# Kernel optimization log

Hardware: AMD Instinct MI355X
Metric: run time of the kernel (lower is better)

## Reference

```python
import jax, jax.numpy as jnp
import numpy as np

N_NODES = 30000


def gcn_conv(x, src, dst, ew, W, b, n):
    # x: [N, Fin] -> linear first (PyG GCNConv), then normalized scatter-add
    h = x @ W  # [N, Fout]
    loops = jnp.arange(n, dtype=src.dtype)
    s = jnp.concatenate([src, loops])
    d = jnp.concatenate([dst, loops])
    w = jnp.concatenate([ew, jnp.ones((n,), dtype=ew.dtype)])
    deg = jax.ops.segment_sum(w, d, num_segments=n)
    dinv = jnp.where(deg > 0, jax.lax.rsqrt(jnp.where(deg > 0, deg, 1.0)), 0.0)
    norm = dinv[s] * w * dinv[d]  # [E+N]
    msg = h[s] * norm[:, None]  # [E+N, Fout]
    out = jax.ops.segment_sum(msg, d, num_segments=n)
    return out + b


def setup_inputs() -> dict:
    key = jax.random.key(0)
    ks = jax.random.split(key, 16)
    n, e, f, c = N_NODES, 480000, 64, 64
    dims = [f, 2 * c, 4 * c, 8 * c]  # 64 -> 128 -> 256 -> 512
    num_classes = 40

    def lin(k, fi, fo):
        k1, k2 = jax.random.split(k)
        s = 1.0 / np.sqrt(fi)
        return (jax.random.uniform(k1, (fi, fo), jnp.float32, -s, s),
                jax.random.uniform(k2, (fo,), jnp.float32, -s, s))

    W1, b1 = lin(ks[0], dims[0], dims[1])
    W2, b2 = lin(ks[1], dims[1], dims[2])
    W3, b3 = lin(ks[2], dims[2], dims[3])
    fW1, fb1 = lin(ks[3], dims[3], dims[3])
    fW2, fb2 = lin(ks[4], dims[3], num_classes)
    return {
        "x": jax.random.normal(ks[5], (n, f), jnp.float32),
        "edge_index": jax.random.randint(ks[6], (2, e), 0, n, jnp.int32),
        "edge_attr": jax.random.uniform(ks[7], (e, 1), jnp.float32),
        "W1": W1, "b1": b1, "W2": W2, "b2": b2, "W3": W3, "b3": b3,
        "fW1": fW1, "fb1": fb1, "fW2": fW2, "fb2": fb2,
    }


def reference(x, edge_index, edge_attr, W1, b1, W2, b2, W3, b3, fW1, fb1, fW2, fb2):
    n = x.shape[0]
    src, dst = edge_index[0], edge_index[1]
    ew = edge_attr.squeeze(-1)
    h = jax.nn.relu(gcn_conv(x, src, dst, ew, W1, b1, n))
    h = jax.nn.relu(gcn_conv(h, src, dst, ew, W2, b2, n))
    h = jax.nn.relu(gcn_conv(h, src, dst, ew, W3, b3, n))
    h = jax.nn.relu(h @ fW1 + fb1)
    h = h @ fW2 + fb2
    return jax.nn.log_softmax(h, axis=1)
```

## Files before the change

### kernel.cpp

```cpp
#include <hip/hip_runtime.h>
#include <cstdint>
#include <cstddef>


typedef _Float16 f16;
typedef _Float16 half8 __attribute__((ext_vector_type(8)));
typedef _Float16 half4 __attribute__((ext_vector_type(4)));
typedef float v4f __attribute__((ext_vector_type(4)));
typedef unsigned long long u64;

__device__ inline void gload_lds16(const void* g, void* l) {
    __builtin_amdgcn_global_load_lds(
        (const __attribute__((address_space(1))) unsigned int*)g,
        (__attribute__((address_space(3))) unsigned int*)l, 16, 0, 0);
}


__global__ __launch_bounds__(256) void k_edge1(const int* __restrict__ dst, const float* __restrict__ ew,
                                               u64* __restrict__ packed, int* __restrict__ eslot, int E) {
    int t = blockIdx.x * blockDim.x + threadIdx.x;
    int e0 = t * 4;
    if (e0 + 3 < E) {
        int4 d4 = *(const int4*)(dst + e0);
        float4 w4 = *(const float4*)(ew + e0);
        u64 a0 = ((u64)__float2uint_rn(w4.x * 1048576.f) << 24) | 1ULL;
        u64 a1 = ((u64)__float2uint_rn(w4.y * 1048576.f) << 24) | 1ULL;
        u64 a2 = ((u64)__float2uint_rn(w4.z * 1048576.f) << 24) | 1ULL;
        u64 a3 = ((u64)__float2uint_rn(w4.w * 1048576.f) << 24) | 1ULL;
        u64 o0 = atomicAdd(&packed[d4.x], a0);
        u64 o1 = atomicAdd(&packed[d4.y], a1);
        u64 o2 = atomicAdd(&packed[d4.z], a2);
        u64 o3 = atomicAdd(&packed[d4.w], a3);
        int4 s;
        s.x = (int)(o0 & 0xFFFFFF); s.y = (int)(o1 & 0xFFFFFF);
        s.z = (int)(o2 & 0xFFFFFF); s.w = (int)(o3 & 0xFFFFFF);
        *(int4*)(eslot + e0) = s;
    } else {
        for (int e = e0; e < E; ++e) {
            u64 a = ((u64)__float2uint_rn(ew[e] * 1048576.f) << 24) | 1ULL;
            u64 o = atomicAdd(&packed[dst[e]], a);
            eslot[e] = (int)(o & 0xFFFFFF);
        }
    }
}

__global__ __launch_bounds__(256) void k_dinv_scan1(const u64* __restrict__ packed,
                                                    float* __restrict__ dinv, int* __restrict__ cnt,
                                                    int* __restrict__ bsum, int n) {
    int i = blockIdx.x * 256 + threadIdx.x;
    int c = 0;
    if (i < n) {
        u64 pk = packed[i];
        c = (int)(pk & 0xFFFFFF);
        float d = 1.0f + (float)(pk >> 24) * (1.0f / 1048576.f);
        float r = rsqrtf(d);
        r = r * (1.5f - 0.5f * d * r * r);
        dinv[i] = r;
        cnt[i] = c;
    }
    int v = c;
#pragma unroll
    for (int o = 32; o; o >>= 1) v += __shfl_xor(v, o);
    __shared__ int s[4];
    if ((threadIdx.x & 63) == 0) s[threadIdx.x >> 6] = v;
    __syncthreads();
    if (threadIdx.x == 0) bsum[blockIdx.x] = s[0] + s[1] + s[2] + s[3];
}

__device__ inline int block_scan_incl(int v) {
    __shared__ int ws[4];
    int lane = threadIdx.x & 63, w = threadIdx.x >> 6;
#pragma unroll
    for (int off = 1; off < 64; off <<= 1) {
        int t = __shfl_up(v, off);
        if (lane >= off) v += t;
    }
    if (lane == 63) ws[w] = v;
    __syncthreads();
    int add = 0;
#pragma unroll
    for (int i = 0; i < 4; ++i) add += (i < w) ? ws[i] : 0;
    __syncthreads();
    return v + add;
}

__global__ __launch_bounds__(256) void k_scan23(const int* __restrict__ cnt, const int* __restrict__ bsum,
                                                int* __restrict__ rowptr, int n, int E) {
    int blk = blockIdx.x, tid = threadIdx.x;
    int i = blk * 256 + tid;
    __shared__ int spre;
    if (tid < 64) {
        int s = 0;
        for (int j = tid; j < blk; j += 64) s += bsum[j];
#pragma unroll
        for (int o = 32; o; o >>= 1) s += __shfl_xor(s, o);
        if (tid == 0) spre = s;
    }
    __syncthreads();
    int v = (i < n) ? cnt[i] : 0;
    int incl = block_scan_incl(v);
    if (i < n) rowptr[i] = spre + incl - v;
    if (i == n - 1) rowptr[n] = E;
}

__global__ __launch_bounds__(256) void k_fill(const int* __restrict__ src, const int* __restrict__ dst,
                                              const float* __restrict__ ew, const int* __restrict__ eslot,
                                              const float* __restrict__ dinv, const int* __restrict__ rowptr,
                                              int* __restrict__ csr_src, float* __restrict__ csr_norm, int E) {
    int e = blockIdx.x * blockDim.x + threadIdx.x;
    if (e < E) {
        int d = dst[e], s = src[e];
        int idx = rowptr[d] + eslot[e];
        csr_src[idx] = s;
        csr_norm[idx] = dinv[s] * ew[e] * dinv[d];
    }
}

struct PrepArgs {
    u64* packed; int n;
    const float* x; f16* xh; int xt4;
    const float* W[5]; f16* WT[5];
    int lgK[5]; int N[5]; int off[6];
};
__global__ __launch_bounds__(256) void k_prep(PrepArgs a) {
    int i = blockIdx.x * 256 + threadIdx.x;
    if (i < a.n) { a.packed[i] = 0ULL; return; }
    int j = i - a.n;
    if (j < a.xt4) {
        float4 v = *(const float4*)(a.x + (size_t)j * 4);
        half4 h = {(f16)v.x, (f16)v.y, (f16)v.z, (f16)v.w};
        *(half4*)(a.xh + (size_t)j * 4) = h;
        return;
    }
    int w = j - a.xt4;
#pragma unroll
    for (int s = 0; s < 5; ++s) {
        if (w >= a.off[s] && w < a.off[s + 1]) {
            int li = w - a.off[s];
            int K = 1 << a.lgK[s];
            int nr = li >> a.lgK[s], k = li & (K - 1);
            float v = (nr < a.N[s]) ? a.W[s][(size_t)k * a.N[s] + nr] : 0.f;
            a.WT[s][li] = (f16)v;
        }
    }
}

template <int F>
__global__ __launch_bounds__(256) void k_agg(const f16* __restrict__ h,
                                             const float* __restrict__ dinv, const int* __restrict__ rowptr,
                                             const int* __restrict__ csr_src, const float* __restrict__ csr_norm,
                                             f16* __restrict__ o, int n) {
    constexpr int LPN = F / 8;
    constexpr int NPW = 64 / LPN;
    int wave = (int)((blockIdx.x * (unsigned)blockDim.x + threadIdx.x) >> 6);
    int lane = threadIdx.x & 63;
    int grp = lane / LPN, lin = lane % LPN;
    int node = wave * NPW + grp;
    if (node >= n) return;
    float di = dinv[node], w0 = di * di;
    float acc[8];
#pragma unroll
    for (int i = 0; i < 8; ++i) acc[i] = 0.f;

    auto gat = [&](int s, float w) {
        half8 x = *(const half8*)(h + (size_t)s * F + lin * 8);
#pragma unroll
        for (int i = 0; i < 8; ++i) acc[i] += w * (float)x[i];
    };

    gat(node, w0);
    int beg = rowptr[node], end = rowptr[node + 1];
    int j = beg;
    for (; j + 3 < end; j += 4) {
        int s0 = csr_src[j], s1 = csr_src[j + 1], s2 = csr_src[j + 2], s3 = csr_src[j + 3];
        float u0 = csr_norm[j], u1 = csr_norm[j + 1], u2 = csr_norm[j + 2], u3 = csr_norm[j + 3];
        gat(s0, u0); gat(s1, u1); gat(s2, u2); gat(s3, u3);
    }
    for (; j < end; ++j) gat(csr_src[j], csr_norm[j]);

    half8 v;
#pragma unroll
    for (int i = 0; i < 8; ++i) v[i] = (f16)acc[i];
    *(half8*)(o + (size_t)node * F + (size_t)lin * 8) = v;
}

template <bool RELU>
__global__ __launch_bounds__(256) void k_mm(const f16* __restrict__ A, const f16* __restrict__ BT,
                                            const float* __restrict__ bias, f16* __restrict__ Ch,
                                            int M, int N, int K, int nB, int nwg) {
    __shared__ f16 lsA[2][128 * 64];
    __shared__ f16 lsB[2][128 * 64];
    int wg = blockIdx.x;
    int q = nwg >> 3, r = nwg & 7;
    int xcd = wg & 7, lin = wg >> 3;
    int wgs = (xcd < r) ? (xcd * (q + 1) + lin) : (r * (q + 1) + (xcd - r) * q + lin);
    int bm = wgs / nB, bn = wgs % nB;

    int tid = threadIdx.x;
    int lane = tid & 63, wid = tid >> 6;
    int l16 = lane & 15, lhi = lane >> 4;
    int wm = (wid >> 1) * 64, wn = (wid & 1) * 64;
    int brow = bm * 128, bcol = bn * 128;

    v4f acc[4][4] = {};

    auto stageA = [&](int buf, int k0) {
#pragma unroll
        for (int it = 0; it < 4; ++it) {
            int b = it * 4096 + tid * 16;
            int row = b >> 7;
            int s = ((b >> 4) & 7) ^ (row & 7);
            gload_lds16(A + (size_t)(brow + row) * K + k0 + s * 8, ((char*)&lsA[buf][0]) + b);
        }
    };
    auto stageB = [&](int buf, int k0) {
#pragma unroll
        for (int it = 0; it < 4; ++it) {
            int b = it * 4096 + tid * 16;
            int row = b >> 7;
            int s = ((b >> 4) & 7) ^ (row & 7);
            gload_lds16(BT + (size_t)(bcol + row) * K + k0 + s * 8, ((char*)&lsB[buf][0]) + b);
        }
    };

    int nk = K >> 6;
    stageA(0, 0);
    stageB(0, 0);
    for (int kt = 0; kt < nk; ++kt) {
        int cur = kt & 1;
        __syncthreads();
        if (kt + 1 < nk) { stageA(cur ^ 1, (kt + 1) << 6); stageB(cur ^ 1, (kt + 1) << 6); }
#pragma unroll
        for (int ks = 0; ks < 2; ++ks) {
            half8 bf[4];
#pragma unroll
            for (int fn = 0; fn < 4; ++fn) {
                int row = wn + fn * 16 + l16;
                int sidx = (ks * 4 + lhi) ^ (row & 7);
                bf[fn] = *(const half8*)(&lsB[cur][0] + row * 64 + sidx * 8);
            }
#pragma unroll
            for (int fm = 0; fm < 4; ++fm) {
                int row = wm + fm * 16 + l16;
                int sidx = (ks * 4 + lhi) ^ (row & 7);
                half8 af = *(const half8*)(&lsA[cur][0] + row * 64 + sidx * 8);
#pragma unroll
                for (int fn = 0; fn < 4; ++fn)
                    acc[fm][fn] = __builtin_amdgcn_mfma_f32_16x16x32_f16(bf[fn], af, acc[fm][fn], 0, 0, 0);
            }
        }
    }
#pragma unroll
    for (int fm = 0; fm < 4; ++fm) {
        int m = brow + wm + fm * 16 + l16;
        if (m >= M) continue;
#pragma unroll
        for (int fn = 0; fn < 4; ++fn) {
            int nb = bcol + wn + fn * 16 + lhi * 4;
            v4f bv = *(const v4f*)(bias + nb);
            v4f v = acc[fm][fn] + bv;
            if (RELU) {
#pragma unroll
                for (int rr = 0; rr < 4; ++rr) v[rr] = fmaxf(v[rr], 0.f);
            }
            half4 hv = {(f16)v[0], (f16)v[1], (f16)v[2], (f16)v[3]};
            *(half4*)(Ch + (size_t)m * N + nb) = hv;
        }
    }
}

template <bool RELU>
__global__ __launch_bounds__(512, 2) void k_mm8(const f16* __restrict__ A, const f16* __restrict__ BT,
                                                const float* __restrict__ bias, f16* __restrict__ Ch,
                                                int M, int N, int K, int nB, int nwg) {
    __shared__ f16 lsA[2][256 * 64];
    __shared__ f16 lsB[2][256 * 64];
    int wg = blockIdx.x;
    int q = nwg >> 3, r = nwg & 7;
    int xcd = wg & 7, lin = wg >> 3;
    int wgs = (xcd < r) ? (xcd * (q + 1) + lin) : (r * (q + 1) + (xcd - r) * q + lin);
    int bm = wgs / nB, bn = wgs % nB;

    int tid = threadIdx.x;
    int lane = tid & 63, wid = tid >> 6;
    int l16 = lane & 15, lhi = lane >> 4;
    int wm = (wid >> 2) * 128, wn = (wid & 3) * 64;
    int brow = bm * 256, bcol = bn * 256;

    v4f acc[8][4] = {};

    auto stageA = [&](int buf, int k0) {
#pragma unroll
        for (int it = 0; it < 4; ++it) {
            int b = it * 8192 + tid * 16;
            int row = b >> 7;
            int s = ((b >> 4) & 7) ^ (row & 7);
            gload_lds16(A + (size_t)(brow + row) * K + k0 + s * 8, ((char*)&lsA[buf][0]) + b);
        }
    };
    auto stageB = [&](int buf, int k0) {
#pragma unroll
        for (int it = 0; it < 4; ++it) {
            int b = it * 8192 + tid * 16;
            int row = b >> 7;
            int s = ((b >> 4) & 7) ^ (row & 7);
            gload_lds16(BT + (size_t)(bcol + row) * K + k0 + s * 8, ((char*)&lsB[buf][0]) + b);
        }
    };

    int nk = K >> 6;
    stageA(0, 0);
    stageB(0, 0);
    for (int kt = 0; kt < nk; ++kt) {
        int cur = kt & 1;
        __syncthreads();
        if (kt + 1 < nk) { stageA(cur ^ 1, (kt + 1) << 6); stageB(cur ^ 1, (kt + 1) << 6); }
#pragma unroll
        for (int ks = 0; ks < 2; ++ks) {
            half8 bf[4];
#pragma unroll
            for (int fn = 0; fn < 4; ++fn) {
                int row = wn + fn * 16 + l16;
                int sidx = (ks * 4 + lhi) ^ (row & 7);
                bf[fn] = *(const half8*)(&lsB[cur][0] + row * 64 + sidx * 8);
            }
#pragma unroll
            for (int fm = 0; fm < 8; ++fm) {
                int row = wm + fm * 16 + l16;
                int sidx = (ks * 4 + lhi) ^ (row & 7);
                half8 af = *(const half8*)(&lsA[cur][0] + row * 64 + sidx * 8);
#pragma unroll
                for (int fn = 0; fn < 4; ++fn)
                    acc[fm][fn] = __builtin_amdgcn_mfma_f32_16x16x32_f16(bf[fn], af, acc[fm][fn], 0, 0, 0);
            }
        }
    }
#pragma unroll
    for (int fm = 0; fm < 8; ++fm) {
        int m = brow + wm + fm * 16 + l16;
        if (m >= M) continue;
#pragma unroll
        for (int fn = 0; fn < 4; ++fn) {
            int nb = bcol + wn + fn * 16 + lhi * 4;
            v4f bv = *(const v4f*)(bias + nb);
            v4f v = acc[fm][fn] + bv;
            if (RELU) {
#pragma unroll
                for (int rr = 0; rr < 4; ++rr) v[rr] = fmaxf(v[rr], 0.f);
            }
            half4 hv = {(f16)v[0], (f16)v[1], (f16)v[2], (f16)v[3]};
            *(half4*)(Ch + (size_t)m * N + nb) = hv;
        }
    }
}

__global__ __launch_bounds__(256) void k_mmfc2(const f16* __restrict__ A, const f16* __restrict__ BT,
                                               const float* __restrict__ bias, float* __restrict__ out,
                                               int M, int K) {
    __shared__ f16 lsA[2][256 * 64];
    __shared__ f16 lsB[2][64 * 64];
    int bm = blockIdx.x;
    int tid = threadIdx.x;
    int lane = tid & 63, wid = tid >> 6;
    int l16 = lane & 15, lhi = lane >> 4;
    int wm = wid * 64;
    int brow = bm * 256;

    v4f acc[4][4] = {};

    auto stageA = [&](int buf, int k0) {
#pragma unroll
        for (int it = 0; it < 8; ++it) {
            int b = it * 4096 + tid * 16;
            int row = b >> 7;
            int s = ((b >> 4) & 7) ^ (row & 7);
            gload_lds16(A + (size_t)(brow + row) * K + k0 + s * 8, ((char*)&lsA[buf][0]) + b);
        }
    };
    auto stageB = [&](int buf, int k0) {
#pragma unroll
        for (int it = 0; it < 2; ++it) {
            int b = it * 4096 + tid * 16;
            int row = b >> 7;
            int s = ((b >> 4) & 7) ^ (row & 7);
            gload_lds16(BT + (size_t)row * K + k0 + s * 8, ((char*)&lsB[buf][0]) + b);
        }
    };

    int nk = K >> 6;
    stageA(0, 0);
    stageB(0, 0);
    for (int kt = 0; kt < nk; ++kt) {
        int cur = kt & 1;
        __syncthreads();
        if (kt + 1 < nk) { stageA(cur ^ 1, (kt + 1) << 6); stageB(cur ^ 1, (kt + 1) << 6); }
#pragma unroll
        for (int ks = 0; ks < 2; ++ks) {
            half8 bf[4];
#pragma unroll
            for (int fn = 0; fn < 4; ++fn) {
                int row = fn * 16 + l16;
                int sidx = (ks * 4 + lhi) ^ (row & 7);
                bf[fn] = *(const half8*)(&lsB[cur][0] + row * 64 + sidx * 8);
            }
#pragma unroll
            for (int fm = 0; fm < 4; ++fm) {
                int row = wm + fm * 16 + l16;
                int sidx = (ks * 4 + lhi) ^ (row & 7);
                half8 af = *(const half8*)(&lsA[cur][0] + row * 64 + sidx * 8);
#pragma unroll
                for (int fn = 0; fn < 4; ++fn)
                    acc[fm][fn] = __builtin_amdgcn_mfma_f32_16x16x32_f16(bf[fn], af, acc[fm][fn], 0, 0, 0);
            }
        }
    }

    float bv[4][4];
#pragma unroll
    for (int fn = 0; fn < 4; ++fn)
#pragma unroll
        for (int rr = 0; rr < 4; ++rr) {
            int nn = fn * 16 + lhi * 4 + rr;
            bv[fn][rr] = (nn < 40) ? bias[nn] : 0.f;
        }

#pragma unroll
    for (int fm = 0; fm < 4; ++fm) {
        int m = brow + wm + fm * 16 + l16;
        float v[4][4];
        float mx = -INFINITY;
#pragma unroll
        for (int fn = 0; fn < 4; ++fn)
#pragma unroll
            for (int rr = 0; rr < 4; ++rr) {
                int nn = fn * 16 + lhi * 4 + rr;
                v[fn][rr] = acc[fm][fn][rr] + bv[fn][rr];
                if (nn < 40) mx = fmaxf(mx, v[fn][rr]);
            }
        mx = fmaxf(mx, __shfl_xor(mx, 16));
        mx = fmaxf(mx, __shfl_xor(mx, 32));
        float s = 0.f;
#pragma unroll
        for (int fn = 0; fn < 3; ++fn)
#pragma unroll
            for (int rr = 0; rr < 4; ++rr) {
                int nn = fn * 16 + lhi * 4 + rr;
                if (nn < 40) s += __expf(v[fn][rr] - mx);
            }
        s += __shfl_xor(s, 16);
        s += __shfl_xor(s, 32);
        float ls = __logf(s);
        if (m < M) {
#pragma unroll
            for (int fn = 0; fn < 3; ++fn)
#pragma unroll
                for (int rr = 0; rr < 4; ++rr) {
                    int nn = fn * 16 + lhi * 4 + rr;
                    if (nn < 40) out[(size_t)m * 40 + nn] = v[fn][rr] - mx - ls;
                }
        }
    }
}


extern "C" void kernel_launch(void* const* d_in, const int* in_sizes, int n_in,
                              void* d_out, int out_size, void* d_ws, size_t ws_size,
                              hipStream_t stream) {
    const float* x   = (const float*)d_in[0];
    const int*   ei  = (const int*)d_in[1];
    const float* ea  = (const float*)d_in[2];
    const float* W1  = (const float*)d_in[3];  const float* b1  = (const float*)d_in[4];
    const float* W2  = (const float*)d_in[5];  const float* b2  = (const float*)d_in[6];
    const float* W3  = (const float*)d_in[7];  const float* b3  = (const float*)d_in[8];
    const float* fW1 = (const float*)d_in[9];  const float* fb1 = (const float*)d_in[10];
    const float* fW2 = (const float*)d_in[11]; const float* fb2 = (const float*)d_in[12];

    int n = in_sizes[0] / 64;
    int E = in_sizes[1] / 2;
    int Mpad = ((n + 255) / 256) * 256;
    const int* src = ei;
    const int* dst = ei + E;
    float* out = (float*)d_out;

    char* p = (char*)d_ws;
    auto alloc = [&](size_t bytes) -> char* {
        char* r = p;
        p += (bytes + 255) & ~(size_t)255;
        return r;
    };
    int nb256 = (n + 255) / 256;
    u64*   packed   = (u64*)alloc((size_t)n * 8);
    float* dinv     = (float*)alloc((size_t)n * 4);
    int*   cnt      = (int*)alloc((size_t)n * 4);
    int*   rowptr   = (int*)alloc((size_t)(n + 1) * 4);
    int*   bsum     = (int*)alloc((size_t)nb256 * 4);
    int*   eslot    = (int*)alloc((size_t)E * 4);
    int*   csr_src  = (int*)alloc((size_t)E * 4);
    float* csr_norm = (float*)alloc((size_t)E * 4);
    f16* XH  = (f16*)alloc((size_t)Mpad * 64 * 2);
    f16* W1T = (f16*)alloc((size_t)128 * 64 * 2);
    f16* W2T = (f16*)alloc((size_t)256 * 128 * 2);
    f16* W3T = (f16*)alloc((size_t)512 * 256 * 2);
    f16* F1T = (f16*)alloc((size_t)512 * 512 * 2);
    f16* F2T = (f16*)alloc((size_t)64 * 512 * 2);
    f16* AGG = (f16*)alloc((size_t)Mpad * 256 * 2);
    f16* HA  = (f16*)alloc((size_t)Mpad * 512 * 2);
    f16* HB  = (f16*)alloc((size_t)Mpad * 512 * 2);

    const int tb = 256;
    int eB = (E + tb - 1) / tb;
    int e4B = (E / 4 + tb - 1) / tb + 1;
    auto aggB = [&](int npw) {
        long waves = (n + npw - 1) / npw;
        return (int)((waves * 64 + tb - 1) / tb);
    };

    {
        PrepArgs a;
        a.packed = packed; a.n = n;
        a.x = x; a.xh = XH; a.xt4 = n * 16;
        a.W[0] = W1;  a.WT[0] = W1T; a.lgK[0] = 6; a.N[0] = 128;
        a.W[1] = W2;  a.WT[1] = W2T; a.lgK[1] = 7; a.N[1] = 256;
        a.W[2] = W3;  a.WT[2] = W3T; a.lgK[2] = 8; a.N[2] = 512;
        a.W[3] = fW1; a.WT[3] = F1T; a.lgK[3] = 9; a.N[3] = 512;
        a.W[4] = fW2; a.WT[4] = F2T; a.lgK[4] = 9; a.N[4] = 40;
        a.off[0] = 0;
        a.off[1] = a.off[0] + 128 * 64;
        a.off[2] = a.off[1] + 256 * 128;
        a.off[3] = a.off[2] + 512 * 256;
        a.off[4] = a.off[3] + 512 * 512;
        a.off[5] = a.off[4] + 64 * 512;
        int tot = a.n + a.xt4 + a.off[5];
        k_prep<<<(tot + tb - 1) / tb, tb, 0, stream>>>(a);
    }

    k_edge1<<<e4B, tb, 0, stream>>>(dst, ea, packed, eslot, E);
    k_dinv_scan1<<<nb256, tb, 0, stream>>>(packed, dinv, cnt, bsum, n);
    k_scan23<<<nb256, tb, 0, stream>>>(cnt, bsum, rowptr, n, E);
    k_fill<<<eB, tb, 0, stream>>>(src, dst, ea, eslot, dinv, rowptr, csr_src, csr_norm, E);

    auto mm8 = [&](const f16* a, const f16* bt, const float* bias, f16* ch, int N, int K) {
        int nB2 = N / 256;
        int nwg = (Mpad / 256) * nB2;
        k_mm8<true><<<nwg, 512, 0, stream>>>(a, bt, bias, ch, n, N, K, nB2, nwg);
    };

    k_agg<64><<<aggB(8), tb, 0, stream>>>(XH, dinv, rowptr, csr_src, csr_norm, AGG, n);
    {
        int nwg = Mpad / 128;
        k_mm<true><<<nwg, 256, 0, stream>>>(AGG, W1T, b1, HA, n, 128, 64, 1, nwg);
    }
    k_agg<128><<<aggB(4), tb, 0, stream>>>(HA, dinv, rowptr, csr_src, csr_norm, AGG, n);
    mm8(AGG, W2T, b2, HB, 256, 128);
    k_agg<256><<<aggB(2), tb, 0, stream>>>(HB, dinv, rowptr, csr_src, csr_norm, AGG, n);
    mm8(AGG, W3T, b3, HA, 512, 256);
    mm8(HA, F1T, fb1, HB, 512, 512);
    k_mmfc2<<<Mpad / 256, 256, 0, stream>>>(HB, F2T, fb2, out, n, 512);
}
```

Baseline: 205.0 us.

## Replicate degree counters into four planes to reduce atomic contention

The per-node packed degree/count accumulator becomes four replicated planes, picked by thread index, so the atomics in the edge pass are spread across more addresses. The scan kernel then sums the four planes and writes per-plane base offsets, and the fill kernel adds the plane base to each edge's slot. The aim is less same-address atomic serialization in k_edge1. In exchange it adds four times the zeroing work and extra reads, plus an int4 gather per edge in the fill kernel.

```diff
diff --git a/kernel.cpp b/kernel.cpp
--- a/kernel.cpp
+++ b/kernel.cpp
@@ -17,9 +17,12 @@
 
 
 __global__ __launch_bounds__(256) void k_edge1(const int* __restrict__ dst, const float* __restrict__ ew,
-                                               u64* __restrict__ packed, int* __restrict__ eslot, int E) {
+                                               u64* __restrict__ packed4, int* __restrict__ eslot,
+                                               int E, int n) {
     int t = blockIdx.x * blockDim.x + threadIdx.x;
     int e0 = t * 4;
+    int r = t & 3;
+    u64* plane = packed4 + (size_t)r * n;
     if (e0 + 3 < E) {
         int4 d4 = *(const int4*)(dst + e0);
         float4 w4 = *(const float4*)(ew + e0);
@@ -27,10 +30,10 @@
         u64 a1 = ((u64)__float2uint_rn(w4.y * 1048576.f) << 24) | 1ULL;
         u64 a2 = ((u64)__float2uint_rn(w4.z * 1048576.f) << 24) | 1ULL;
         u64 a3 = ((u64)__float2uint_rn(w4.w * 1048576.f) << 24) | 1ULL;
-        u64 o0 = atomicAdd(&packed[d4.x], a0);
-        u64 o1 = atomicAdd(&packed[d4.y], a1);
-        u64 o2 = atomicAdd(&packed[d4.z], a2);
-        u64 o3 = atomicAdd(&packed[d4.w], a3);
+        u64 o0 = atomicAdd(&plane[d4.x], a0);
+        u64 o1 = atomicAdd(&plane[d4.y], a1);
+        u64 o2 = atomicAdd(&plane[d4.z], a2);
+        u64 o3 = atomicAdd(&plane[d4.w], a3);
         int4 s;
         s.x = (int)(o0 & 0xFFFFFF); s.y = (int)(o1 & 0xFFFFFF);
         s.z = (int)(o2 & 0xFFFFFF); s.w = (int)(o3 & 0xFFFFFF);
@@ -38,21 +41,27 @@
     } else {
         for (int e = e0; e < E; ++e) {
             u64 a = ((u64)__float2uint_rn(ew[e] * 1048576.f) << 24) | 1ULL;
-            u64 o = atomicAdd(&packed[dst[e]], a);
+            u64 o = atomicAdd(&plane[dst[e]], a);
             eslot[e] = (int)(o & 0xFFFFFF);
         }
     }
 }
 
-__global__ __launch_bounds__(256) void k_dinv_scan1(const u64* __restrict__ packed,
+__global__ __launch_bounds__(256) void k_dinv_scan1(const u64* __restrict__ packed4,
                                                     float* __restrict__ dinv, int* __restrict__ cnt,
-                                                    int* __restrict__ bsum, int n) {
+                                                    int4* __restrict__ rbase, int* __restrict__ bsum, int n) {
     int i = blockIdx.x * 256 + threadIdx.x;
     int c = 0;
     if (i < n) {
-        u64 pk = packed[i];
-        c = (int)(pk & 0xFFFFFF);
-        float d = 1.0f + (float)(pk >> 24) * (1.0f / 1048576.f);
+        u64 p0 = packed4[i];
+        u64 p1 = packed4[(size_t)n + i];
+        u64 p2 = packed4[(size_t)2 * n + i];
+        u64 p3 = packed4[(size_t)3 * n + i];
+        int c0 = (int)(p0 & 0xFFFFFF), c1 = (int)(p1 & 0xFFFFFF);
+        int c2 = (int)(p2 & 0xFFFFFF), c3 = (int)(p3 & 0xFFFFFF);
+        c = c0 + c1 + c2 + c3;
+        rbase[i] = make_int4(0, c0, c0 + c1, c0 + c1 + c2);
+        float d = 1.0f + (float)((p0 >> 24) + (p1 >> 24) + (p2 >> 24) + (p3 >> 24)) * (1.0f / 1048576.f);
         float r = rsqrtf(d);
         r = r * (1.5f - 0.5f * d * r * r);
         dinv[i] = r;
@@ -106,26 +115,30 @@
 __global__ __launch_bounds__(256) void k_fill(const int* __restrict__ src, const int* __restrict__ dst,
                                               const float* __restrict__ ew, const int* __restrict__ eslot,
                                               const float* __restrict__ dinv, const int* __restrict__ rowptr,
+                                              const int4* __restrict__ rbase,
                                               int* __restrict__ csr_src, float* __restrict__ csr_norm, int E) {
     int e = blockIdx.x * blockDim.x + threadIdx.x;
     if (e < E) {
         int d = dst[e], s = src[e];
-        int idx = rowptr[d] + eslot[e];
+        int r = (e >> 2) & 3;
+        int4 rb = rbase[d];
+        int base = (r == 0) ? rb.x : (r == 1) ? rb.y : (r == 2) ? rb.z : rb.w;
+        int idx = rowptr[d] + base + eslot[e];
         csr_src[idx] = s;
         csr_norm[idx] = dinv[s] * ew[e] * dinv[d];
     }
 }
 
 struct PrepArgs {
-    u64* packed; int n;
+    u64* packed4; int n4;
     const float* x; f16* xh; int xt4;
     const float* W[5]; f16* WT[5];
     int lgK[5]; int N[5]; int off[6];
 };
 __global__ __launch_bounds__(256) void k_prep(PrepArgs a) {
     int i = blockIdx.x * 256 + threadIdx.x;
-    if (i < a.n) { a.packed[i] = 0ULL; return; }
-    int j = i - a.n;
+    if (i < a.n4) { a.packed4[i] = 0ULL; return; }
+    int j = i - a.n4;
     if (j < a.xt4) {
         float4 v = *(const float4*)(a.x + (size_t)j * 4);
         half4 h = {(f16)v.x, (f16)v.y, (f16)v.z, (f16)v.w};
@@ -489,9 +502,10 @@
         return r;
     };
     int nb256 = (n + 255) / 256;
-    u64*   packed   = (u64*)alloc((size_t)n * 8);
+    u64*   packed4  = (u64*)alloc((size_t)n * 4 * 8);
     float* dinv     = (float*)alloc((size_t)n * 4);
     int*   cnt      = (int*)alloc((size_t)n * 4);
+    int4*  rbase    = (int4*)alloc((size_t)n * 16);
     int*   rowptr   = (int*)alloc((size_t)(n + 1) * 4);
     int*   bsum     = (int*)alloc((size_t)nb256 * 4);
     int*   eslot    = (int*)alloc((size_t)E * 4);
@@ -517,7 +531,7 @@
 
     {
         PrepArgs a;
-        a.packed = packed; a.n = n;
+        a.packed4 = packed4; a.n4 = n * 4;
         a.x = x; a.xh = XH; a.xt4 = n * 16;
         a.W[0] = W1;  a.WT[0] = W1T; a.lgK[0] = 6; a.N[0] = 128;
         a.W[1] = W2;  a.WT[1] = W2T; a.lgK[1] = 7; a.N[1] = 256;
@@ -530,14 +544,14 @@
         a.off[3] = a.off[2] + 512 * 256;
         a.off[4] = a.off[3] + 512 * 512;
         a.off[5] = a.off[4] + 64 * 512;
-        int tot = a.n + a.xt4 + a.off[5];
+        int tot = a.n4 + a.xt4 + a.off[5];
         k_prep<<<(tot + tb - 1) / tb, tb, 0, stream>>>(a);
     }
 
-    k_edge1<<<e4B, tb, 0, stream>>>(dst, ea, packed, eslot, E);
-    k_dinv_scan1<<<nb256, tb, 0, stream>>>(packed, dinv, cnt, bsum, n);
+    k_edge1<<<e4B, tb, 0, stream>>>(dst, ea, packed4, eslot, E, n);
+    k_dinv_scan1<<<nb256, tb, 0, stream>>>(packed4, dinv, cnt, rbase, bsum, n);
     k_scan23<<<nb256, tb, 0, stream>>>(cnt, bsum, rowptr, n, E);
-    k_fill<<<eB, tb, 0, stream>>>(src, dst, ea, eslot, dinv, rowptr, csr_src, csr_norm, E);
+    k_fill<<<eB, tb, 0, stream>>>(src, dst, ea, eslot, dinv, rowptr, rbase, csr_src, csr_norm, E);
 
     auto mm8 = [&](const f16* a, const f16* bt, const float* bias, f16* ch, int N, int K) {
         int nB2 = N / 256;
```

Result: no change. 205.9 us (+0.4%).
